# Kernel tuning notes

Hardware: AMD Instinct MI355X
Metric: run time of the kernel (lower is better)

## Reference

```python
import jax, jax.numpy as jnp
import numpy as np

REG = 0.1
EPS = 2.220446049250313e-16  # np.finfo(float).eps, cast to working dtype


def setup_inputs() -> dict:
    key = jax.random.key(0)
    k1, k2, k3 = jax.random.split(key, 3)
    x = jax.random.normal(k1, (262144, 512), dtype=jnp.float32)
    w = jax.random.normal(k2, (512,), dtype=jnp.float32)
    b = jax.random.normal(k3, (1,), dtype=jnp.float32)
    return {"x": x, "w": w, "b": b}


def reference(x, w, b):
    # net(x): [N, D] @ [D] + b -> [N]
    out = x @ w + b[0]
    n = out.shape[0]
    # sum(pdist(out[:, None], p=1)) == sum over i<j of |out_i - out_j|.
    # Exact sort-based closed form: with s sorted ascending,
    #   sum_{i<j}(s_j - s_i) = sum_i (2i - (n-1)) * s_i
    s = jnp.sort(out)
    coef = 2.0 * jnp.arange(n, dtype=out.dtype) - jnp.asarray(n - 1, out.dtype)
    pair_sum = jnp.sum(coef * s)
    loss = -jnp.sum(out) + (REG / n) * pair_sum
    # heaviside(out, zero_pos=True) = relu(sign(out + eps)); prod -> verified flag
    is_verified = jnp.prod(jax.nn.relu(jnp.sign(out + jnp.asarray(EPS, out.dtype))))
    return loss, is_verified
```

## Files before the change

kernel.cpp:

```cpp
#include <hip/hip_runtime.h>
#include <stdint.h>
#include <stddef.h>

#define NBINS 65536
#define EPSF 2.220446049250313e-16f
#define RTILE 4096

__device__ __forceinline__ uint32_t f2key(float f) {
    uint32_t u = __float_as_uint(f);
    return (u & 0x80000000u) ? ~u : (u | 0x80000000u);
}
__device__ __forceinline__ float key2f(uint32_t k) {
    uint32_t u = (k & 0x80000000u) ? (k ^ 0x80000000u) : ~k;
    return __uint_as_float(u);
}

__global__ __launch_bounds__(256) void gemv_kernel(
    const float* __restrict__ x, const float* __restrict__ w,
    const float* __restrict__ bptr, uint32_t* __restrict__ keys,
    int N, int D, double* __restrict__ sum_out, int* __restrict__ bad_flag)
{
    __shared__ float4 w4s[512];
    const int tid = threadIdx.x;
    const int nf4 = D >> 2;
    const float4* w4g = (const float4*)w;
    for (int i = tid; i < nf4; i += 256) w4s[i] = w4g[i];
    __syncthreads();

    const int wave = tid >> 6, lane = tid & 63;
    const int gwave0 = blockIdx.x * 4 + wave;
    const int nwaves = gridDim.x * 4;
    const float b0 = bptr[0];

    double lsum = 0.0;
    int lbad = 0;
    for (int row = gwave0; row < N; row += nwaves) {
        const float4* xr = (const float4*)(x + (size_t)row * D);
        float dot = 0.f;
        for (int i = lane; i < nf4; i += 64) {
            float4 a = xr[i];
            float4 bb = w4s[i];
            dot = fmaf(a.x, bb.x, dot);
            dot = fmaf(a.y, bb.y, dot);
            dot = fmaf(a.z, bb.z, dot);
            dot = fmaf(a.w, bb.w, dot);
        }
        #pragma unroll
        for (int off = 32; off > 0; off >>= 1) dot += __shfl_down(dot, off, 64);
        if (lane == 0) {
            float f = dot + b0;
            keys[row] = f2key(f);
            lsum += (double)f;
            lbad |= (f + EPSF > 0.f) ? 0 : 1;
        }
    }

    __shared__ double sd[4];
    __shared__ int si[4];
    if (lane == 0) { sd[wave] = lsum; si[wave] = lbad; }
    __syncthreads();
    if (tid == 0) {
        atomicAdd(sum_out, sd[0] + sd[1] + sd[2] + sd[3]);
        int bd = si[0] | si[1] | si[2] | si[3];
        if (bd) atomicOr(bad_flag, 1);
    }
}

__global__ __launch_bounds__(256) void hist_kernel(
    const uint32_t* __restrict__ keys, uint32_t* __restrict__ hist, int N)
{
    int i = blockIdx.x * 256 + threadIdx.x;
    if (i < N) atomicAdd(&hist[keys[i] >> 16], 1u);
}

__global__ __launch_bounds__(1024) void scan_kernel(
    const uint32_t* __restrict__ hist, uint32_t* __restrict__ base,
    uint32_t* __restrict__ cnt)
{
    __shared__ uint32_t partial[1024];
    const int t = threadIdx.x;
    const int per = NBINS / 1024;
    uint32_t s = 0;
    for (int i = 0; i < per; ++i) s += hist[t * per + i];
    partial[t] = s;
    __syncthreads();
    for (int off = 1; off < 1024; off <<= 1) {
        uint32_t v = (t >= off) ? partial[t - off] : 0u;
        __syncthreads();
        partial[t] += v;
        __syncthreads();
    }
    uint32_t run = (t == 0) ? 0u : partial[t - 1];
    for (int i = 0; i < per; ++i) {
        int idx = t * per + i;
        base[idx] = run;
        cnt[idx] = run;
        run += hist[idx];
    }
    if (t == 1023) base[NBINS] = run;
}

__global__ __launch_bounds__(256) void scatter_kernel(
    const uint32_t* __restrict__ keys, uint32_t* __restrict__ cnt,
    uint32_t* __restrict__ sorted, int N)
{
    int i = blockIdx.x * 256 + threadIdx.x;
    if (i < N) {
        uint32_t k = keys[i];
        uint32_t pos = atomicAdd(&cnt[k >> 16], 1u);
        sorted[pos] = k;
    }
}

__global__ __launch_bounds__(256) void rank_kernel(
    const uint32_t* __restrict__ sorted, const uint32_t* __restrict__ base,
    int N, double* __restrict__ pairpart)
{
    const int b = blockIdx.x;
    const uint32_t start = base[b], end = base[b + 1];
    const uint32_t m = end - start;
    if (m == 0) return;

    __shared__ uint32_t tile[RTILE];
    const int tid = threadIdx.x;
    double acc = 0.0;
    const uint32_t rounds = (m + 255u) / 256u;
    for (uint32_t r = 0; r < rounds; ++r) {
        uint32_t p = start + r * 256u + (uint32_t)tid;
        bool active = (p < end);
        uint32_t k = active ? sorted[p] : 0u;
        uint32_t lc = 0, eq = 0;
        for (uint32_t ts = start; ts < end; ts += RTILE) {
            uint32_t tn = end - ts;
            if (tn > RTILE) tn = RTILE;
            __syncthreads();
            for (uint32_t j = (uint32_t)tid; j < tn; j += 256u) tile[j] = sorted[ts + j];
            __syncthreads();
            if (active) {
                for (uint32_t j = 0; j < tn; ++j) {
                    uint32_t kk = tile[j];
                    lc += (kk < k) ? 1u : 0u;
                    eq += (kk == k) ? 1u : 0u;
                }
            }
        }
        if (active) {
            float f = key2f(k);
            double coef = 2.0 * (double)(start + lc) + (double)eq - (double)N;
            acc += coef * (double)f;
        }
    }

    __shared__ double sred[256];
    sred[tid] = acc;
    __syncthreads();
    for (int off = 128; off > 0; off >>= 1) {
        if (tid < off) sred[tid] += sred[tid + off];
        __syncthreads();
    }
    if (tid == 0) pairpart[b] = sred[0];
}

__global__ __launch_bounds__(1024) void finalize_kernel(
    const double* __restrict__ pairpart, const double* __restrict__ sum_out,
    const int* __restrict__ bad_flag, float* __restrict__ out, int N)
{
    __shared__ double sred[1024];
    const int t = threadIdx.x;
    double s = 0.0;
    for (int i = t; i < NBINS; i += 1024) s += pairpart[i];
    sred[t] = s;
    __syncthreads();
    for (int off = 512; off > 0; off >>= 1) {
        if (t < off) sred[t] += sred[t + off];
        __syncthreads();
    }
    if (t == 0) {
        double loss = -sum_out[0] + (0.1 / (double)N) * sred[0];
        out[0] = (float)loss;
        out[1] = bad_flag[0] ? 0.0f : 1.0f;
    }
}

extern "C" void kernel_launch(void* const* d_in, const int* in_sizes, int n_in,
                              void* d_out, int out_size, void* d_ws, size_t ws_size,
                              hipStream_t stream) {
    (void)n_in; (void)out_size; (void)ws_size;
    const float* x = (const float*)d_in[0];
    const float* w = (const float*)d_in[1];
    const float* b = (const float*)d_in[2];
    float* out = (float*)d_out;
    const int D = in_sizes[1];
    const int N = in_sizes[0] / D;

    uint8_t* W = (uint8_t*)d_ws;
    uint32_t* hist     = (uint32_t*)(W);
    double*   pairpart = (double*)(W + 262144);
    double*   sum_out  = (double*)(W + 786432);
    int*      bad_flag = (int*)(W + 786440);
    uint32_t* base     = (uint32_t*)(W + 786448);
    uint32_t* cnt      = (uint32_t*)(W + 1048600);
    uint32_t* keys     = (uint32_t*)(W + 1310744);
    uint32_t* sorted   = (uint32_t*)(W + 1310744 + (size_t)N * 4);

    hipMemsetAsync(d_ws, 0, 786448, stream);
    gemv_kernel<<<2048, 256, 0, stream>>>(x, w, b, keys, N, D, sum_out, bad_flag);
    hist_kernel<<<(N + 255) / 256, 256, 0, stream>>>(keys, hist, N);
    scan_kernel<<<1, 1024, 0, stream>>>(hist, base, cnt);
    scatter_kernel<<<(N + 255) / 256, 256, 0, stream>>>(keys, cnt, sorted, N);
    rank_kernel<<<NBINS, 256, 0, stream>>>(sorted, base, N, pairpart);
    finalize_kernel<<<1, 1024, 0, stream>>>(pairpart, sum_out, bad_flag, out, N);
}
```

Measured before the change: 987.0 us.

## Fuse histogram into GEMV, compact nonempty bins, persistent rank kernel with fused finalize

Moves the histogram atomics into the GEMV epilogue, which drops the separate hist kernel. GEMV rows are now assigned to waves as contiguous chunks rather than strided. The scan builds a compacted list of nonempty bins so rank_kernel can run as a persistent 2048-block grid over only the occupied bins. Bins that fit in one tile are loaded once into LDS and scanned with vectorized uint4 compares. Finalize is folded into the last block via an atomic done counter, which removes two launches and the 65536-block grid. The cost is extra global atomics in GEMV and a serialized last-block completion step.

After: 985.5 us. Within noise of the previous version (-0.2%).

```diff
diff --git a/kernel.cpp b/kernel.cpp
--- a/kernel.cpp
+++ b/kernel.cpp
@@ -18,7 +18,8 @@
 __global__ __launch_bounds__(256) void gemv_kernel(
     const float* __restrict__ x, const float* __restrict__ w,
     const float* __restrict__ bptr, uint32_t* __restrict__ keys,
-    int N, int D, double* __restrict__ sum_out, int* __restrict__ bad_flag)
+    uint32_t* __restrict__ hist, int N, int D,
+    double* __restrict__ sum_out, int* __restrict__ bad_flag)
 {
     __shared__ float4 w4s[512];
     const int tid = threadIdx.x;
@@ -28,13 +29,16 @@
     __syncthreads();
 
     const int wave = tid >> 6, lane = tid & 63;
-    const int gwave0 = blockIdx.x * 4 + wave;
+    const int gwave = blockIdx.x * 4 + wave;
     const int nwaves = gridDim.x * 4;
+    const int rows_per = (N + nwaves - 1) / nwaves;
+    const int r0 = gwave * rows_per;
+    const int r1 = (r0 + rows_per < N) ? (r0 + rows_per) : N;
     const float b0 = bptr[0];
 
     double lsum = 0.0;
     int lbad = 0;
-    for (int row = gwave0; row < N; row += nwaves) {
+    for (int row = r0; row < r1; ++row) {
         const float4* xr = (const float4*)(x + (size_t)row * D);
         float dot = 0.f;
         for (int i = lane; i < nf4; i += 64) {
@@ -49,7 +53,9 @@
         for (int off = 32; off > 0; off >>= 1) dot += __shfl_down(dot, off, 64);
         if (lane == 0) {
             float f = dot + b0;
-            keys[row] = f2key(f);
+            uint32_t k = f2key(f);
+            keys[row] = k;
+            atomicAdd(&hist[k >> 16], 1u);
             lsum += (double)f;
             lbad |= (f + EPSF > 0.f) ? 0 : 1;
         }
@@ -66,19 +72,15 @@
     }
 }
 
-__global__ __launch_bounds__(256) void hist_kernel(
-    const uint32_t* __restrict__ keys, uint32_t* __restrict__ hist, int N)
-{
-    int i = blockIdx.x * 256 + threadIdx.x;
-    if (i < N) atomicAdd(&hist[keys[i] >> 16], 1u);
-}
-
 __global__ __launch_bounds__(1024) void scan_kernel(
     const uint32_t* __restrict__ hist, uint32_t* __restrict__ base,
-    uint32_t* __restrict__ cnt)
+    uint32_t* __restrict__ cnt, uint32_t* __restrict__ nzb,
+    int* __restrict__ nb_count)
 {
     __shared__ uint32_t partial[1024];
+    __shared__ int nb_lds;
     const int t = threadIdx.x;
+    if (t == 0) nb_lds = 0;
     const int per = NBINS / 1024;
     uint32_t s = 0;
     for (int i = 0; i < per; ++i) s += hist[t * per + i];
@@ -93,11 +95,18 @@
     uint32_t run = (t == 0) ? 0u : partial[t - 1];
     for (int i = 0; i < per; ++i) {
         int idx = t * per + i;
+        uint32_t h = hist[idx];
         base[idx] = run;
         cnt[idx] = run;
-        run += hist[idx];
+        if (h != 0u) {
+            int pos = atomicAdd(&nb_lds, 1);
+            nzb[pos] = (uint32_t)idx;
+        }
+        run += h;
     }
     if (t == 1023) base[NBINS] = run;
+    __syncthreads();
+    if (t == 0) *nb_count = nb_lds;
 }
 
 __global__ __launch_bounds__(256) void scatter_kernel(
@@ -114,71 +123,97 @@
 
 __global__ __launch_bounds__(256) void rank_kernel(
     const uint32_t* __restrict__ sorted, const uint32_t* __restrict__ base,
-    int N, double* __restrict__ pairpart)
-{
-    const int b = blockIdx.x;
-    const uint32_t start = base[b], end = base[b + 1];
-    const uint32_t m = end - start;
-    if (m == 0) return;
-
+    const uint32_t* __restrict__ nzb, const int* __restrict__ nb_count,
+    int N, double* __restrict__ pair_acc, const double* __restrict__ sum_out,
+    const int* __restrict__ bad_flag, int* __restrict__ done_cnt,
+    float* __restrict__ out)
+{
     __shared__ uint32_t tile[RTILE];
+    __shared__ double sred[256];
     const int tid = threadIdx.x;
+    const int nb = *nb_count;
     double acc = 0.0;
-    const uint32_t rounds = (m + 255u) / 256u;
-    for (uint32_t r = 0; r < rounds; ++r) {
-        uint32_t p = start + r * 256u + (uint32_t)tid;
-        bool active = (p < end);
-        uint32_t k = active ? sorted[p] : 0u;
-        uint32_t lc = 0, eq = 0;
-        for (uint32_t ts = start; ts < end; ts += RTILE) {
-            uint32_t tn = end - ts;
-            if (tn > RTILE) tn = RTILE;
+
+    for (int ib = blockIdx.x; ib < nb; ib += gridDim.x) {
+        const uint32_t b = nzb[ib];
+        const uint32_t start = base[b], end = base[b + 1];
+        const uint32_t m = end - start;
+
+        if (m <= RTILE) {
             __syncthreads();
-            for (uint32_t j = (uint32_t)tid; j < tn; j += 256u) tile[j] = sorted[ts + j];
+            for (uint32_t j = tid; j < m; j += 256u) tile[j] = sorted[start + j];
             __syncthreads();
-            if (active) {
-                for (uint32_t j = 0; j < tn; ++j) {
-                    uint32_t kk = tile[j];
-                    lc += (kk < k) ? 1u : 0u;
-                    eq += (kk == k) ? 1u : 0u;
+            const uint32_t rounds = (m + 255u) / 256u;
+            for (uint32_t r = 0; r < rounds; ++r) {
+                uint32_t p = r * 256u + (uint32_t)tid;
+                if (p < m) {
+                    uint32_t k = tile[p];
+                    uint32_t lc = 0, eq = 0;
+                    uint32_t m4 = m & ~3u, j = 0;
+                    for (; j < m4; j += 4) {
+                        uint4 t4 = *(const uint4*)(tile + j);
+                        lc += (t4.x < k); eq += (t4.x == k);
+                        lc += (t4.y < k); eq += (t4.y == k);
+                        lc += (t4.z < k); eq += (t4.z == k);
+                        lc += (t4.w < k); eq += (t4.w == k);
+                    }
+                    for (; j < m; ++j) {
+                        uint32_t kk = tile[j];
+                        lc += (kk < k); eq += (kk == k);
+                    }
+                    double coef = 2.0 * (double)(start + lc) + (double)eq - (double)N;
+                    acc += coef * (double)key2f(k);
                 }
             }
-        }
-        if (active) {
-            float f = key2f(k);
-            double coef = 2.0 * (double)(start + lc) + (double)eq - (double)N;
-            acc += coef * (double)f;
-        }
-    }
-
-    __shared__ double sred[256];
+        } else {
+            const uint32_t rounds = (m + 255u) / 256u;
+            for (uint32_t r = 0; r < rounds; ++r) {
+                uint32_t p = start + r * 256u + (uint32_t)tid;
+                bool active = (p < end);
+                uint32_t k = active ? sorted[p] : 0u;
+                uint32_t lc = 0, eq = 0;
+                for (uint32_t ts = start; ts < end; ts += RTILE) {
+                    uint32_t tn = end - ts;
+                    if (tn > RTILE) tn = RTILE;
+                    __syncthreads();
+                    for (uint32_t j = tid; j < tn; j += 256u) tile[j] = sorted[ts + j];
+                    __syncthreads();
+                    if (active) {
+                        for (uint32_t j = 0; j < tn; ++j) {
+                            uint32_t kk = tile[j];
+                            lc += (kk < k); eq += (kk == k);
+                        }
+                    }
+                }
+                if (active) {
+                    double coef = 2.0 * (double)(start + lc) + (double)eq - (double)N;
+                    acc += coef * (double)key2f(k);
+                }
+            }
+        }
+    }
+
     sred[tid] = acc;
     __syncthreads();
     for (int off = 128; off > 0; off >>= 1) {
         if (tid < off) sred[tid] += sred[tid + off];
         __syncthreads();
     }
-    if (tid == 0) pairpart[b] = sred[0];
-}
-
-__global__ __launch_bounds__(1024) void finalize_kernel(
-    const double* __restrict__ pairpart, const double* __restrict__ sum_out,
-    const int* __restrict__ bad_flag, float* __restrict__ out, int N)
-{
-    __shared__ double sred[1024];
-    const int t = threadIdx.x;
-    double s = 0.0;
-    for (int i = t; i < NBINS; i += 1024) s += pairpart[i];
-    sred[t] = s;
-    __syncthreads();
-    for (int off = 512; off > 0; off >>= 1) {
-        if (t < off) sred[t] += sred[t + off];
-        __syncthreads();
-    }
-    if (t == 0) {
-        double loss = -sum_out[0] + (0.1 / (double)N) * sred[0];
-        out[0] = (float)loss;
-        out[1] = bad_flag[0] ? 0.0f : 1.0f;
+    if (tid == 0) {
+        if (sred[0] != 0.0) atomicAdd(pair_acc, sred[0]);
+        __threadfence();
+        int d = atomicAdd(done_cnt, 1);
+        if (d == (int)gridDim.x - 1) {
+            __threadfence();
+            double pp = __longlong_as_double(
+                atomicAdd((unsigned long long*)pair_acc, 0ULL));
+            double so = __longlong_as_double(
+                atomicAdd((unsigned long long*)const_cast<double*>(sum_out), 0ULL));
+            int bd = atomicAdd(const_cast<int*>(bad_flag), 0);
+            double loss = -so + (0.1 / (double)N) * pp;
+            out[0] = (float)loss;
+            out[1] = bd ? 0.0f : 1.0f;
+        }
     }
 }
 
@@ -195,19 +230,21 @@
 
     uint8_t* W = (uint8_t*)d_ws;
     uint32_t* hist     = (uint32_t*)(W);
-    double*   pairpart = (double*)(W + 262144);
-    double*   sum_out  = (double*)(W + 786432);
-    int*      bad_flag = (int*)(W + 786440);
-    uint32_t* base     = (uint32_t*)(W + 786448);
-    uint32_t* cnt      = (uint32_t*)(W + 1048600);
-    uint32_t* keys     = (uint32_t*)(W + 1310744);
-    uint32_t* sorted   = (uint32_t*)(W + 1310744 + (size_t)N * 4);
-
-    hipMemsetAsync(d_ws, 0, 786448, stream);
-    gemv_kernel<<<2048, 256, 0, stream>>>(x, w, b, keys, N, D, sum_out, bad_flag);
-    hist_kernel<<<(N + 255) / 256, 256, 0, stream>>>(keys, hist, N);
-    scan_kernel<<<1, 1024, 0, stream>>>(hist, base, cnt);
+    double*   sum_out  = (double*)(W + 262144);
+    double*   pair_acc = (double*)(W + 262152);
+    int*      bad_flag = (int*)(W + 262160);
+    int*      done_cnt = (int*)(W + 262164);
+    int*      nb_count = (int*)(W + 262168);
+    uint32_t* base     = (uint32_t*)(W + 262176);
+    uint32_t* cnt      = (uint32_t*)(W + 524336);
+    uint32_t* nzb      = (uint32_t*)(W + 786480);
+    uint32_t* keys     = (uint32_t*)(W + 1048624);
+    uint32_t* sorted   = keys + N;
+
+    hipMemsetAsync(d_ws, 0, 262176, stream);
+    gemv_kernel<<<2048, 256, 0, stream>>>(x, w, b, keys, hist, N, D, sum_out, bad_flag);
+    scan_kernel<<<1, 1024, 0, stream>>>(hist, base, cnt, nzb, nb_count);
     scatter_kernel<<<(N + 255) / 256, 256, 0, stream>>>(keys, cnt, sorted, N);
-    rank_kernel<<<NBINS, 256, 0, stream>>>(sorted, base, N, pairpart);
-    finalize_kernel<<<1, 1024, 0, stream>>>(pairpart, sum_out, bad_flag, out, N);
-}
+    rank_kernel<<<2048, 256, 0, stream>>>(sorted, base, nzb, nb_count, N,
+                                          pair_acc, sum_out, bad_flag, done_cnt, out);
+}
```
